# Kernel optimization log

Measured on AMD Instinct MI355X. Metric: run time of the kernel, lower is better.

## Reference

```python
import jax, jax.numpy as jnp
import numpy as np

N = 100_000      # nodes
E = 1_600_000    # edges (avg degree 16)
D = 64           # input_dim
H = 64           # hidden_dim
G = 2048         # graphs in batch
EPS = 1e-5       # BatchNorm eps


def setup_inputs() -> dict:
    key = jax.random.key(0)
    ks = jax.random.split(key, 12)
    x = jax.random.normal(ks[0], (N, D), dtype=jnp.float32)
    edge_index = jax.random.randint(ks[1], (2, E), 0, N, dtype=jnp.int64)
    batch = jnp.sort(jax.random.randint(ks[2], (N,), 0, G, dtype=jnp.int64))
    s = 1.0 / np.sqrt(D)
    W1 = jax.random.normal(ks[3], (D, H), dtype=jnp.float32) * s
    b1 = jnp.zeros((H,), jnp.float32)
    g1 = jnp.ones((H,), jnp.float32)
    bt1 = jnp.zeros((H,), jnp.float32)
    W2 = jax.random.normal(ks[4], (H, H), dtype=jnp.float32) * s
    b2 = jnp.zeros((H,), jnp.float32)
    g2 = jnp.ones((H,), jnp.float32)
    bt2 = jnp.zeros((H,), jnp.float32)
    return {"x": x, "edge_index": edge_index, "batch": batch,
            "W1": W1, "b1": b1, "g1": g1, "bt1": bt1,
            "W2": W2, "b2": b2, "g2": g2, "bt2": bt2,
            "num_graphs": G}


def reference(x, edge_index, batch, W1, b1, g1, bt1, W2, b2, g2, bt2, num_graphs):
    n = x.shape[0]
    # GCN normalization with added self-loops (PyG GCNConv default)
    loops = jnp.arange(n, dtype=edge_index.dtype)
    src = jnp.concatenate([edge_index[0], loops])
    dst = jnp.concatenate([edge_index[1], loops])
    deg = jax.ops.segment_sum(jnp.ones(src.shape, jnp.float32), dst, num_segments=n)
    dis = jax.lax.rsqrt(jnp.maximum(deg, 1.0))  # deg >= 1 with self-loops
    norm = dis[src] * dis[dst]                  # [E+N]

    def gcn(h, W, b):
        h = h @ W                               # [N,H] dense transform first
        msg = h[src] * norm[:, None]            # gather + scale  [E+N, H]
        return jax.ops.segment_sum(msg, dst, num_segments=n) + b

    def bn(h, gamma, beta):
        mu = h.mean(axis=0)
        var = h.var(axis=0)
        return (h - mu) * jax.lax.rsqrt(var + EPS) * gamma + beta

    h = jax.nn.relu(bn(gcn(x, W1, b1), g1, bt1))
    h = jax.nn.relu(bn(gcn(h, W2, b2), g2, bt2))

    # global mean pool over graph ids
    ones = jnp.ones((n,), jnp.float32)
    counts = jax.ops.segment_sum(ones, batch, num_segments=num_graphs)
    sums = jax.ops.segment_sum(h, batch, num_segments=num_graphs)
    return sums / jnp.maximum(counts, 1.0)[:, None]
```

## Files before the change

### kernel.cpp

```cpp
#include <hip/hip_runtime.h>
#include <hip/hip_bf16.h>

#define BN_EPS 1e-5f
#define CCHUNK 8192

__device__ __forceinline__ float bf2f(ushort u) {
    return __uint_as_float(((unsigned int)u) << 16);
}
__device__ __forceinline__ ushort f2bf(float f) {
    unsigned int u = __float_as_uint(f);
    u += 0x7FFFu + ((u >> 16) & 1u);
    return (ushort)(u >> 16);
}

__global__ void k_bhist(const int* __restrict__ dst, int E, int nb, int* __restrict__ bktcnt) {
    __shared__ int lh[1024];
    for (int j = threadIdx.x; j < nb; j += 256) lh[j] = 0;
    __syncthreads();
    for (int i = blockIdx.x * blockDim.x + threadIdx.x; i < E; i += gridDim.x * blockDim.x)
        atomicAdd(&lh[dst[i] >> 7], 1);
    __syncthreads();
    for (int j = threadIdx.x; j < nb; j += 256) {
        int c = lh[j];
        if (c) atomicAdd(&bktcnt[j], c);
    }
}

__global__ void k_bscan(const int* __restrict__ bktcnt, int nb, int N,
                        int* __restrict__ bktoff, int* __restrict__ gpos,
                        int* __restrict__ rowptr) {
    __shared__ int sh[256];
    int tid = threadIdx.x;
    int base = tid * 4;
    int v[4]; int tsum = 0;
    #pragma unroll
    for (int k = 0; k < 4; ++k) {
        int i = base + k;
        v[k] = (i < nb) ? bktcnt[i] : 0;
        tsum += v[k];
    }
    sh[tid] = tsum;
    __syncthreads();
    for (int off = 1; off < 256; off <<= 1) {
        int add = (tid >= off) ? sh[tid - off] : 0;
        __syncthreads();
        sh[tid] += add;
        __syncthreads();
    }
    int excl = sh[tid] - tsum;
    #pragma unroll
    for (int k = 0; k < 4; ++k) {
        int i = base + k;
        if (i <= nb) {
            bktoff[i] = excl;
            if (i < nb) gpos[i] = excl;
        }
        excl += v[k];
    }
    if (tid == 255) rowptr[N] = sh[255];
}

__global__ void k_partition(const int* __restrict__ src, const int* __restrict__ dst,
                            int E, int nb, int sb,
                            int* __restrict__ gpos, unsigned int* __restrict__ eb) {
    __shared__ int lh[1024];
    int e0 = blockIdx.x * CCHUNK;
    int cnt = min(CCHUNK, E - e0);
    for (int j = threadIdx.x; j < nb; j += 256) lh[j] = 0;
    __syncthreads();
    for (int k = threadIdx.x; k < cnt; k += 256)
        atomicAdd(&lh[dst[e0 + k] >> 7], 1);
    __syncthreads();
    for (int j = threadIdx.x; j < nb; j += 256) {
        int c = lh[j];
        if (c) lh[j] = atomicAdd(&gpos[j], c);
    }
    __syncthreads();
    for (int k = threadIdx.x; k < cnt; k += 256) {
        int d = dst[e0 + k];
        unsigned int s = (unsigned int)src[e0 + k];
        int pos = atomicAdd(&lh[d >> 7], 1);
        eb[pos] = (((unsigned int)(d & 127)) << sb) | s;
    }
}

__global__ void k_row(const unsigned int* __restrict__ eb, const int* __restrict__ bktoff,
                      int sb, int N, float* __restrict__ dis, int* __restrict__ rowptr) {
    __shared__ int h[128];
    __shared__ int p[128];
    int tid = threadIdx.x;
    int b = blockIdx.x;
    if (tid < 128) h[tid] = 0;
    __syncthreads();
    int e0 = bktoff[b], e1 = bktoff[b + 1];
    for (int e = e0 + tid; e < e1; e += 256)
        atomicAdd(&h[(eb[e] >> sb) & 127], 1);
    __syncthreads();
    if (tid < 128) p[tid] = h[tid];
    __syncthreads();
    for (int off = 1; off < 128; off <<= 1) {
        int add = (tid < 128 && tid >= off) ? p[tid - off] : 0;
        __syncthreads();
        if (tid < 128) p[tid] += add;
        __syncthreads();
    }
    if (tid < 128) {
        int d = b * 128 + tid;
        if (d < N) {
            rowptr[d] = e0 + p[tid] - h[tid];
            dis[d] = rsqrtf((float)(h[tid] + 1));
        }
    }
}

__global__ void k_csrfill(const unsigned int* __restrict__ eb, const int* __restrict__ bktoff,
                          const int* __restrict__ rowptr, int sb, unsigned int smask,
                          int N, int* __restrict__ cs) {
    __shared__ int nc[128];
    int tid = threadIdx.x;
    int b = blockIdx.x;
    if (tid < 128) {
        int d = b * 128 + tid;
        nc[tid] = (d < N) ? rowptr[d] : 0;
    }
    __syncthreads();
    int e0 = bktoff[b], e1 = bktoff[b + 1];
    for (int e = e0 + tid; e < e1; e += 256) {
        unsigned int v = eb[e];
        int dl = (v >> sb) & 127;
        int slot = atomicAdd(&nc[dl], 1);
        cs[slot] = (int)(v & smask);
    }
}

__global__ void k_matmul64t(const float* __restrict__ X, const float* __restrict__ W,
                            const float* __restrict__ bnp, int n, ushort* __restrict__ tb) {
    __shared__ float Xs[64][68];
    __shared__ float Ws[64][64];
    const int tid = threadIdx.x;
    const int rowbase = blockIdx.x * 64;

    {
        const float4* W4 = (const float4*)W;
        float4* Ws4 = (float4*)&Ws[0][0];
        #pragma unroll
        for (int k = 0; k < 4; ++k) Ws4[tid + 256 * k] = W4[tid + 256 * k];
    }
    {
        const int r  = tid >> 2;
        const int c0 = (tid & 3) * 16;
        const int row = rowbase + r;
        #pragma unroll
        for (int j = 0; j < 4; ++j) {
            float4 v;
            if (row < n) v = *(const float4*)&X[(size_t)row * 64 + c0 + 4 * j];
            else v = make_float4(0.f, 0.f, 0.f, 0.f);
            float vv[4] = {v.x, v.y, v.z, v.w};
            #pragma unroll
            for (int i = 0; i < 4; ++i) {
                int c = c0 + 4 * j + i;
                float f = vv[i];
                if (bnp) f = fmaxf(0.f, fmaf(f, bnp[c], bnp[64 + c]));
                Xs[c][r] = f;
            }
        }
    }
    __syncthreads();

    const int r0 = (tid & 15) * 4;
    const int c0 = (tid >> 4) * 4;
    float acc[4][4];
    #pragma unroll
    for (int i = 0; i < 4; ++i)
        #pragma unroll
        for (int j = 0; j < 4; ++j) acc[i][j] = 0.f;

    #pragma unroll 4
    for (int k = 0; k < 64; ++k) {
        float4 xv = *(const float4*)&Xs[k][r0];
        float4 wv = *(const float4*)&Ws[k][c0];
        float xa[4] = {xv.x, xv.y, xv.z, xv.w};
        float wa[4] = {wv.x, wv.y, wv.z, wv.w};
        #pragma unroll
        for (int i = 0; i < 4; ++i)
            #pragma unroll
            for (int j = 0; j < 4; ++j)
                acc[i][j] = fmaf(xa[i], wa[j], acc[i][j]);
    }

    #pragma unroll
    for (int i = 0; i < 4; ++i) {
        int row = rowbase + r0 + i;
        if (row < n) {
            ushort4 o;
            o.x = f2bf(acc[i][0]); o.y = f2bf(acc[i][1]);
            o.z = f2bf(acc[i][2]); o.w = f2bf(acc[i][3]);
            *(ushort4*)&tb[(size_t)row * 64 + c0] = o;
        }
    }
}

__global__ void k_gather(const int* __restrict__ cs, const int* __restrict__ rowptr,
                         const float* __restrict__ dis, const ushort* __restrict__ tb,
                         int n, float* __restrict__ a) {
    int lane = threadIdx.x & 63;
    int wave = threadIdx.x >> 6;
    int row = blockIdx.x * 4 + wave;
    if (row >= n) return;
    const int hl = lane & 15;
    const int q  = lane >> 4;
    int e0 = rowptr[row], e1 = rowptr[row + 1];
    float disrow = dis[row];
    float ax = 0.f, ay = 0.f, az = 0.f, aw = 0.f;
    for (int base = e0; base < e1; base += 64) {
        int cnt = min(64, e1 - base);
        int p = (lane < cnt) ? cs[base + lane] : 0;
        int nq = (cnt + 3) >> 2;
        for (int j = 0; j < nq; ++j) {
            int idx = 4 * j + q;
            int s = __shfl(p, idx);
            float w = (idx < cnt) ? dis[s] * disrow : 0.f;
            ushort4 tv = *(const ushort4*)&tb[(size_t)s * 64 + 4 * hl];
            ax = fmaf(bf2f(tv.x), w, ax);
            ay = fmaf(bf2f(tv.y), w, ay);
            az = fmaf(bf2f(tv.z), w, az);
            aw = fmaf(bf2f(tv.w), w, aw);
        }
    }
    ax += __shfl_xor(ax, 16); ay += __shfl_xor(ay, 16);
    az += __shfl_xor(az, 16); aw += __shfl_xor(aw, 16);
    ax += __shfl_xor(ax, 32); ay += __shfl_xor(ay, 32);
    az += __shfl_xor(az, 32); aw += __shfl_xor(aw, 32);
    if (q == 0) {
        float d2 = disrow * disrow;
        ushort4 ts = *(const ushort4*)&tb[(size_t)row * 64 + 4 * hl];
        ax = fmaf(bf2f(ts.x), d2, ax);
        ay = fmaf(bf2f(ts.y), d2, ay);
        az = fmaf(bf2f(ts.z), d2, az);
        aw = fmaf(bf2f(ts.w), d2, aw);
        *(float4*)&a[(size_t)row * 64 + 4 * hl] = make_float4(ax, ay, az, aw);
    }
}

__global__ void k_stats(const float* __restrict__ a, int n, float* __restrict__ stats) {
    int c = threadIdx.x & 63;
    int grp = threadIdx.x >> 6;
    float s = 0.f, s2 = 0.f;
    for (int r = blockIdx.x * 4 + grp; r < n; r += gridDim.x * 4) {
        float v = a[(size_t)r * 64 + c];
        s += v; s2 += v * v;
    }
    __shared__ float sh[2][4][64];
    sh[0][grp][c] = s; sh[1][grp][c] = s2;
    __syncthreads();
    if (threadIdx.x < 64) {
        float S  = sh[0][0][c] + sh[0][1][c] + sh[0][2][c] + sh[0][3][c];
        float S2 = sh[1][0][c] + sh[1][1][c] + sh[1][2][c] + sh[1][3][c];
        atomicAdd(&stats[c], S);
        atomicAdd(&stats[64 + c], S2);
    }
}

__global__ void k_bnparams(const float* __restrict__ stats, const float* __restrict__ g,
                           const float* __restrict__ bt, int n, float* __restrict__ bnp) {
    int c = threadIdx.x;
    if (c < 64) {
        float inv_n = 1.f / (float)n;
        float mean = stats[c] * inv_n;
        float var = stats[64 + c] * inv_n - mean * mean;
        float s = g[c] * rsqrtf(var + BN_EPS);
        bnp[c] = s;
        bnp[64 + c] = bt[c] - mean * s;
    }
}

__global__ void k_gbound(const int* __restrict__ batch, int n, int G, int* __restrict__ gs) {
    int g = blockIdx.x * blockDim.x + threadIdx.x;
    if (g > G) return;
    int lo = 0, hi = n;
    while (lo < hi) { int mid = (lo + hi) >> 1; if (batch[mid] < g) lo = mid + 1; else hi = mid; }
    gs[g] = lo;
}

__global__ void k_pool2(const float* __restrict__ a, const float* __restrict__ bnp,
                        const int* __restrict__ gs, int G, float* __restrict__ out) {
    int lane = threadIdx.x & 63;
    int wave = threadIdx.x >> 6;
    int g = blockIdx.x * 4 + wave;
    if (g >= G) return;
    int s = gs[g], e = gs[g + 1];
    float sc = bnp[lane], of = bnp[64 + lane];
    float acc = 0.f;
    for (int r = s; r < e; ++r)
        acc += fmaxf(0.f, fmaf(a[(size_t)r * 64 + lane], sc, of));
    out[(size_t)g * 64 + lane] = acc / (float)max(e - s, 1);
}

extern "C" void kernel_launch(void* const* d_in, const int* in_sizes, int n_in,
                              void* d_out, int out_size, void* d_ws, size_t ws_size,
                              hipStream_t stream) {
    const float* x     = (const float*)d_in[0];
    const int*   ei    = (const int*)d_in[1];
    const int*   batch = (const int*)d_in[2];
    const float* W1    = (const float*)d_in[3];
    const float* g1    = (const float*)d_in[5];
    const float* bt1   = (const float*)d_in[6];
    const float* W2    = (const float*)d_in[7];
    const float* g2    = (const float*)d_in[9];
    const float* bt2   = (const float*)d_in[10];

    const int N = in_sizes[0] / 64;
    const int E = in_sizes[1] / 2;
    const int G = out_size / 64;

    const int* src = ei;
    const int* dst = ei + E;

    const int nb = (N + 127) >> 7;
    int sb = 0; while ((1 << sb) < N) ++sb;
    const unsigned int smask = (1u << sb) - 1u;

    ushort* tb        = (ushort*)d_ws;
    float* a          = (float*)(tb + (size_t)N * 64);
    int*   cs         = (int*)(a + (size_t)N * 64);
    unsigned int* eb  = (unsigned int*)(cs + E);
    float* dis        = (float*)(eb + E);
    int*   rowptr     = (int*)(dis + N);
    int*   bktcnt     = rowptr + N + 1;
    int*   bktoff     = bktcnt + nb;
    int*   gpos       = bktoff + nb + 1;
    float* stats      = (float*)(gpos + nb);
    float* bnp        = stats + 128;
    int*   gs         = (int*)(bnp + 128);

    float* out = (float*)d_out;

    const int mmBlocks = (N + 63) / 64;
    const int gaBlocks = (N + 3) / 4;
    const int pcBlocks = (E + CCHUNK - 1) / CCHUNK;

    hipMemsetAsync(bktcnt, 0, (size_t)nb * sizeof(int), stream);
    k_bhist<<<256, 256, 0, stream>>>(dst, E, nb, bktcnt);
    k_bscan<<<1, 256, 0, stream>>>(bktcnt, nb, N, bktoff, gpos, rowptr);
    k_partition<<<pcBlocks, 256, 0, stream>>>(src, dst, E, nb, sb, gpos, eb);
    k_row<<<nb, 256, 0, stream>>>(eb, bktoff, sb, N, dis, rowptr);
    k_csrfill<<<nb, 256, 0, stream>>>(eb, bktoff, rowptr, sb, smask, N, cs);
    k_gbound<<<(G + 256) / 256, 256, 0, stream>>>(batch, N, G, gs);

    k_matmul64t<<<mmBlocks, 256, 0, stream>>>(x, W1, nullptr, N, tb);
    k_gather<<<gaBlocks, 256, 0, stream>>>(cs, rowptr, dis, tb, N, a);
    hipMemsetAsync(stats, 0, 128 * sizeof(float), stream);
    k_stats<<<512, 256, 0, stream>>>(a, N, stats);
    k_bnparams<<<1, 64, 0, stream>>>(stats, g1, bt1, N, bnp);

    k_matmul64t<<<mmBlocks, 256, 0, stream>>>(a, W2, bnp, N, tb);
    k_gather<<<gaBlocks, 256, 0, stream>>>(cs, rowptr, dis, tb, N, a);
    hipMemsetAsync(stats, 0, 128 * sizeof(float), stream);
    k_stats<<<512, 256, 0, stream>>>(a, N, stats);
    k_bnparams<<<1, 64, 0, stream>>>(stats, g2, bt2, N, bnp);

    k_pool2<<<(G + 3) / 4, 256, 0, stream>>>(a, bnp, gs, G, out);
}
```

Baseline: 338.7 us.

## Precompute per-edge GCN weights in CSR and widen gather to 16-byte loads

```diff
diff --git a/kernel.cpp b/kernel.cpp
--- a/kernel.cpp
+++ b/kernel.cpp
@@ -114,22 +114,27 @@
 }
 
 __global__ void k_csrfill(const unsigned int* __restrict__ eb, const int* __restrict__ bktoff,
-                          const int* __restrict__ rowptr, int sb, unsigned int smask,
-                          int N, int* __restrict__ cs) {
+                          const int* __restrict__ rowptr, const float* __restrict__ dis,
+                          int sb, unsigned int smask, int N,
+                          int* __restrict__ cs, float* __restrict__ wf) {
     __shared__ int nc[128];
+    __shared__ float dl[128];
     int tid = threadIdx.x;
     int b = blockIdx.x;
     if (tid < 128) {
         int d = b * 128 + tid;
         nc[tid] = (d < N) ? rowptr[d] : 0;
+        dl[tid] = (d < N) ? dis[d] : 1.f;
     }
     __syncthreads();
     int e0 = bktoff[b], e1 = bktoff[b + 1];
     for (int e = e0 + tid; e < e1; e += 256) {
         unsigned int v = eb[e];
-        int dl = (v >> sb) & 127;
-        int slot = atomicAdd(&nc[dl], 1);
-        cs[slot] = (int)(v & smask);
+        int dloc = (v >> sb) & 127;
+        int s = (int)(v & smask);
+        int slot = atomicAdd(&nc[dloc], 1);
+        cs[slot] = s;
+        wf[slot] = dis[s] * dl[dloc];
     }
 }
 
@@ -200,45 +205,61 @@
     }
 }
 
-__global__ void k_gather(const int* __restrict__ cs, const int* __restrict__ rowptr,
-                         const float* __restrict__ dis, const ushort* __restrict__ tb,
-                         int n, float* __restrict__ a) {
+__global__ void k_gather(const int* __restrict__ cs, const float* __restrict__ wf,
+                         const int* __restrict__ rowptr, const float* __restrict__ dis,
+                         const ushort* __restrict__ tb, int n, float* __restrict__ a) {
     int lane = threadIdx.x & 63;
     int wave = threadIdx.x >> 6;
     int row = blockIdx.x * 4 + wave;
     if (row >= n) return;
-    const int hl = lane & 15;
-    const int q  = lane >> 4;
+    const int fl = lane & 7;
+    const int o  = lane >> 3;
     int e0 = rowptr[row], e1 = rowptr[row + 1];
-    float disrow = dis[row];
-    float ax = 0.f, ay = 0.f, az = 0.f, aw = 0.f;
+    float acc[8];
+    #pragma unroll
+    for (int i = 0; i < 8; ++i) acc[i] = 0.f;
     for (int base = e0; base < e1; base += 64) {
         int cnt = min(64, e1 - base);
-        int p = (lane < cnt) ? cs[base + lane] : 0;
-        int nq = (cnt + 3) >> 2;
+        int   p  = (lane < cnt) ? cs[base + lane] : 0;
+        float wv = (lane < cnt) ? wf[base + lane] : 0.f;
+        int nq = (cnt + 7) >> 3;
         for (int j = 0; j < nq; ++j) {
-            int idx = 4 * j + q;
+            int idx = 8 * j + o;
             int s = __shfl(p, idx);
-            float w = (idx < cnt) ? dis[s] * disrow : 0.f;
-            ushort4 tv = *(const ushort4*)&tb[(size_t)s * 64 + 4 * hl];
-            ax = fmaf(bf2f(tv.x), w, ax);
-            ay = fmaf(bf2f(tv.y), w, ay);
-            az = fmaf(bf2f(tv.z), w, az);
-            aw = fmaf(bf2f(tv.w), w, aw);
-        }
-    }
-    ax += __shfl_xor(ax, 16); ay += __shfl_xor(ay, 16);
-    az += __shfl_xor(az, 16); aw += __shfl_xor(aw, 16);
-    ax += __shfl_xor(ax, 32); ay += __shfl_xor(ay, 32);
-    az += __shfl_xor(az, 32); aw += __shfl_xor(aw, 32);
-    if (q == 0) {
-        float d2 = disrow * disrow;
-        ushort4 ts = *(const ushort4*)&tb[(size_t)row * 64 + 4 * hl];
-        ax = fmaf(bf2f(ts.x), d2, ax);
-        ay = fmaf(bf2f(ts.y), d2, ay);
-        az = fmaf(bf2f(ts.z), d2, az);
-        aw = fmaf(bf2f(ts.w), d2, aw);
-        *(float4*)&a[(size_t)row * 64 + 4 * hl] = make_float4(ax, ay, az, aw);
+            float w = __shfl(wv, idx);
+            uint4 tv = *(const uint4*)&tb[(size_t)s * 64 + 8 * fl];
+            acc[0] = fmaf(__uint_as_float(tv.x << 16),         w, acc[0]);
+            acc[1] = fmaf(__uint_as_float(tv.x & 0xffff0000u), w, acc[1]);
+            acc[2] = fmaf(__uint_as_float(tv.y << 16),         w, acc[2]);
+            acc[3] = fmaf(__uint_as_float(tv.y & 0xffff0000u), w, acc[3]);
+            acc[4] = fmaf(__uint_as_float(tv.z << 16),         w, acc[4]);
+            acc[5] = fmaf(__uint_as_float(tv.z & 0xffff0000u), w, acc[5]);
+            acc[6] = fmaf(__uint_as_float(tv.w << 16),         w, acc[6]);
+            acc[7] = fmaf(__uint_as_float(tv.w & 0xffff0000u), w, acc[7]);
+        }
+    }
+    #pragma unroll
+    for (int i = 0; i < 8; ++i) {
+        acc[i] += __shfl_xor(acc[i], 8);
+        acc[i] += __shfl_xor(acc[i], 16);
+        acc[i] += __shfl_xor(acc[i], 32);
+    }
+    if (o == 0) {
+        float dr = dis[row];
+        float d2 = dr * dr;
+        uint4 ts = *(const uint4*)&tb[(size_t)row * 64 + 8 * fl];
+        acc[0] = fmaf(__uint_as_float(ts.x << 16),         d2, acc[0]);
+        acc[1] = fmaf(__uint_as_float(ts.x & 0xffff0000u), d2, acc[1]);
+        acc[2] = fmaf(__uint_as_float(ts.y << 16),         d2, acc[2]);
+        acc[3] = fmaf(__uint_as_float(ts.y & 0xffff0000u), d2, acc[3]);
+        acc[4] = fmaf(__uint_as_float(ts.z << 16),         d2, acc[4]);
+        acc[5] = fmaf(__uint_as_float(ts.z & 0xffff0000u), d2, acc[5]);
+        acc[6] = fmaf(__uint_as_float(ts.w << 16),         d2, acc[6]);
+        acc[7] = fmaf(__uint_as_float(ts.w & 0xffff0000u), d2, acc[7]);
+        float4 o0 = make_float4(acc[0], acc[1], acc[2], acc[3]);
+        float4 o1 = make_float4(acc[4], acc[5], acc[6], acc[7]);
+        *(float4*)&a[(size_t)row * 64 + 8 * fl]     = o0;
+        *(float4*)&a[(size_t)row * 64 + 8 * fl + 4] = o1;
     }
 }
 
@@ -323,14 +344,15 @@
     ushort* tb        = (ushort*)d_ws;
     float* a          = (float*)(tb + (size_t)N * 64);
     int*   cs         = (int*)(a + (size_t)N * 64);
-    unsigned int* eb  = (unsigned int*)(cs + E);
+    float* wf         = (float*)(cs + E);
+    unsigned int* eb  = (unsigned int*)(wf + E);
     float* dis        = (float*)(eb + E);
     int*   rowptr     = (int*)(dis + N);
     int*   bktcnt     = rowptr + N + 1;
-    int*   bktoff     = bktcnt + nb;
+    float* stats      = (float*)(bktcnt + nb);
+    int*   bktoff     = (int*)(stats + 256);
     int*   gpos       = bktoff + nb + 1;
-    float* stats      = (float*)(gpos + nb);
-    float* bnp        = stats + 128;
+    float* bnp        = (float*)(gpos + nb);
     int*   gs         = (int*)(bnp + 128);
 
     float* out = (float*)d_out;
@@ -339,25 +361,23 @@
     const int gaBlocks = (N + 3) / 4;
     const int pcBlocks = (E + CCHUNK - 1) / CCHUNK;
 
-    hipMemsetAsync(bktcnt, 0, (size_t)nb * sizeof(int), stream);
+    hipMemsetAsync(bktcnt, 0, (size_t)(nb + 256) * sizeof(int), stream);
     k_bhist<<<256, 256, 0, stream>>>(dst, E, nb, bktcnt);
     k_bscan<<<1, 256, 0, stream>>>(bktcnt, nb, N, bktoff, gpos, rowptr);
     k_partition<<<pcBlocks, 256, 0, stream>>>(src, dst, E, nb, sb, gpos, eb);
     k_row<<<nb, 256, 0, stream>>>(eb, bktoff, sb, N, dis, rowptr);
-    k_csrfill<<<nb, 256, 0, stream>>>(eb, bktoff, rowptr, sb, smask, N, cs);
+    k_csrfill<<<nb, 256, 0, stream>>>(eb, bktoff, rowptr, dis, sb, smask, N, cs, wf);
     k_gbound<<<(G + 256) / 256, 256, 0, stream>>>(batch, N, G, gs);
 
     k_matmul64t<<<mmBlocks, 256, 0, stream>>>(x, W1, nullptr, N, tb);
-    k_gather<<<gaBlocks, 256, 0, stream>>>(cs, rowptr, dis, tb, N, a);
-    hipMemsetAsync(stats, 0, 128 * sizeof(float), stream);
+    k_gather<<<gaBlocks, 256, 0, stream>>>(cs, wf, rowptr, dis, tb, N, a);
     k_stats<<<512, 256, 0, stream>>>(a, N, stats);
     k_bnparams<<<1, 64, 0, stream>>>(stats, g1, bt1, N, bnp);
 
     k_matmul64t<<<mmBlocks, 256, 0, stream>>>(a, W2, bnp, N, tb);
-    k_gather<<<gaBlocks, 256, 0, stream>>>(cs, rowptr, dis, tb, N, a);
-    hipMemsetAsync(stats, 0, 128 * sizeof(float), stream);
-    k_stats<<<512, 256, 0, stream>>>(a, N, stats);
-    k_bnparams<<<1, 64, 0, stream>>>(stats, g2, bt2, N, bnp);
+    k_gather<<<gaBlocks, 256, 0, stream>>>(cs, wf, rowptr, dis, tb, N, a);
+    k_stats<<<512, 256, 0, stream>>>(a, N, stats + 128);
+    k_bnparams<<<1, 64, 0, stream>>>(stats + 128, g2, bt2, N, bnp);
 
     k_pool2<<<(G + 3) / 4, 256, 0, stream>>>(a, bnp, gs, G, out);
 }
```

Measured after the change: 304.0 us. -10.2%, faster.
